# Optimization experiments

Hardware: AMD Instinct MI355X
Metric: run time of the kernel (lower is better)

The kernel has to match this reference:

```python
import jax, jax.numpy as jnp
import numpy as np

KSIZE = 11
SIGMA = 1.5
PAD = KSIZE // 2
C1 = 0.01 ** 2
C2 = 0.03 ** 2


def gaussian_kernel(ksize, sigma):
    ax = np.arange(ksize, dtype=np.float32) - (ksize - 1) / 2.0
    g = np.exp(-(ax ** 2) / (2.0 * sigma ** 2))
    k2d = np.outer(g, g)
    k2d = k2d / k2d.sum()
    # depthwise kernel for 3 channels: [out=3, in/groups=1, kh, kw]
    return jnp.asarray(np.broadcast_to(k2d, (3, 1, ksize, ksize)).copy())


def dwconv(x, kernel):
    # x: [B,3,H,W], kernel: [3,1,k,k], 'same' padding, groups=3
    return jax.lax.conv_general_dilated(
        x, kernel,
        window_strides=(1, 1),
        padding=[(PAD, PAD), (PAD, PAD)],
        dimension_numbers=('NCHW', 'OIHW', 'NCHW'),
        feature_group_count=3)


def setup_inputs() -> dict:
    key = jax.random.key(0)
    k1, k2 = jax.random.split(key)
    shape = (16, 3, 512, 512)
    img_output = jax.random.uniform(k1, shape, dtype=jnp.float32)
    img_target = jax.random.uniform(k2, shape, dtype=jnp.float32)
    kernel = gaussian_kernel(KSIZE, SIGMA)
    return {"img_output": img_output, "img_target": img_target, "kernel": kernel}


def reference(img_output, img_target, kernel):
    s, t = img_output, img_target
    ux = dwconv(s, kernel)
    uy = dwconv(t, kernel)
    uxx = dwconv(s * s, kernel)
    uyy = dwconv(t * t, kernel)
    uxy = dwconv(s * t, kernel)
    ssim = ((2 * ux * uy + C1) * (2 * (uxy - ux * uy) + C2)
            / (ux ** 2 + uy ** 2 + C1)
            / (uxx - ux * ux + (uyy - uy * uy) + C2))
    return 1.0 - ssim.mean()
```

## Files before the change

### kernel.cpp

```cpp
#include <hip/hip_runtime.h>

typedef _Float16 f16;
typedef f16  f16x8 __attribute__((ext_vector_type(8)));
typedef f16  f16x2 __attribute__((ext_vector_type(2)));
typedef float f32x4 __attribute__((ext_vector_type(4)));

#define W 512
#define H 512
#define KS 11
#define NW 4
#define NBLK 6144
#define NLINES 256
#define C1_SSIM 0.0001f
#define C2_SSIM 0.0009f
#define NTOTAL 12582912.0f

__device__ __constant__ const float GW[KS] = {
    1.02838e-3f, 7.59876e-3f, 3.600076e-2f, 1.0936069e-1f, 2.1300554e-1f,
    2.6601172e-1f,
    2.1300554e-1f, 1.0936069e-1f, 3.600076e-2f, 7.59876e-3f, 1.02838e-3f
};

union B32 { f16x2 h; int i; };

__device__ inline float ssim_px(float ux, float uy, float uxx, float uyy, float uxy) {
    const float uxuy = ux * uy;
    const float a = 2.f * uxuy + C1_SSIM;
    const float b = 2.f * (uxy - uxuy) + C2_SSIM;
    const float c = ux * ux + uy * uy + C1_SSIM;
    const float d = (uxx - ux * ux) + (uyy - uy * uy) + C2_SSIM;
    return (a * b) * __builtin_amdgcn_rcpf(c * d);
}

struct __attribute__((aligned(4))) F4 { float x, y, z, w; };

__device__ __forceinline__ void load8f(const float* __restrict__ base, int ry,
                                       int xs, float v[8]) {
    if ((unsigned)ry < (unsigned)H) {
        const float* r = base + ((size_t)ry << 9);
        if ((unsigned)xs <= (unsigned)(W - 8)) {
            const F4 a = *(const F4*)(r + xs);
            const F4 b = *(const F4*)(r + xs + 4);
            v[0] = a.x; v[1] = a.y; v[2] = a.z; v[3] = a.w;
            v[4] = b.x; v[5] = b.y; v[6] = b.z; v[7] = b.w;
        } else {
            #pragma unroll
            for (int j = 0; j < 8; ++j) {
                const int x = xs + j;
                v[j] = ((unsigned)x < (unsigned)W) ? r[x] : 0.f;
            }
        }
    } else {
        #pragma unroll
        for (int j = 0; j < 8; ++j) v[j] = 0.f;
    }
}

__device__ __forceinline__ f16x8 pack8(const float v[8]) {
    f16x8 r;
    #pragma unroll
    for (int p = 0; p < 4; ++p) {
        const f16x2 h = __builtin_bit_cast(
            f16x2, __builtin_amdgcn_cvt_pkrtz(v[2 * p], v[2 * p + 1]));
        r[2 * p]     = h[0];
        r[2 * p + 1] = h[1];
    }
    return r;
}

__global__ __launch_bounds__(256, 5)
void ssim_main(const float* __restrict__ simg, const float* __restrict__ timg,
               float* __restrict__ accum) {
    __shared__ float red[NW];

    const int tid  = threadIdx.x;
    const int w    = tid >> 6;
    const int lane = tid & 63;
    const int n    = lane & 15;
    const int q    = lane >> 4;

    const int L  = blockIdx.x * NW + w;
    const int z  = L >> 9;
    const int r  = L & 511;
    const int ty = r >> 5;
    const int tx = r & 31;

    const float* sp = simg + ((size_t)z << 18);
    const float* tp = timg + ((size_t)z << 18);
    const int x0 = tx << 4;
    const int y0 = (ty << 5) - 5;
    const int xs = x0 - 5 + (q << 3);

    f16x8 af;
    #pragma unroll
    for (int j = 0; j < 8; ++j) {
        const int k = (q << 3) + j;
        const int d = k - n;
        af[j] = (d >= 0 && d < KS) ? (f16)GW[d] : (f16)0.f;
    }

    const int LA = n | ((q & 1) << 5);
    const int LB = LA | 16;

    B32 ph[3][5][2];
    #pragma unroll
    for (int g = 0; g < 3; ++g) {
        float v[8];
        load8f(sp, y0 + (g << 4) + n, xs, v);
        const f16x8 sf = pack8(v);
        load8f(tp, y0 + (g << 4) + n, xs, v);
        const f16x8 tf = pack8(v);
        #pragma unroll
        for (int c = 0; c < 5; ++c) {
            f16x8 ch;
            if      (c == 0) ch = sf;
            else if (c == 1) ch = tf;
            else if (c == 2) ch = sf * sf;
            else if (c == 3) ch = tf * tf;
            else             ch = sf * tf;
            const f32x4 zero = {0.f, 0.f, 0.f, 0.f};
            const f32x4 d = __builtin_amdgcn_mfma_f32_16x16x32_f16(ch, af, zero, 0, 0, 0);
            ph[g][c][0].h = __builtin_bit_cast(f16x2, __builtin_amdgcn_cvt_pkrtz(d[0], d[1]));
            ph[g][c][1].h = __builtin_bit_cast(f16x2, __builtin_amdgcn_cvt_pkrtz(d[2], d[3]));
        }
    }

    float sum = 0.f;
    #pragma unroll
    for (int t = 0; t < 2; ++t) {
        f32x4 acc[5];
        #pragma unroll
        for (int c = 0; c < 5; ++c) {
            B32 a0, a1, a2, a3, b0, b1, b2, b3, r0, r1, r2, r3;
            a0.i = __shfl(ph[t][c][0].i,     LA, 64);
            a1.i = __shfl(ph[t][c][1].i,     LA, 64);
            a2.i = __shfl(ph[t][c][0].i,     LB, 64);
            a3.i = __shfl(ph[t][c][1].i,     LB, 64);
            b0.i = __shfl(ph[t + 1][c][0].i, LA, 64);
            b1.i = __shfl(ph[t + 1][c][1].i, LA, 64);
            b2.i = __shfl(ph[t + 1][c][0].i, LB, 64);
            b3.i = __shfl(ph[t + 1][c][1].i, LB, 64);
            const bool lo = (q < 2);
            r0.i = lo ? a0.i : b0.i;
            r1.i = lo ? a1.i : b1.i;
            r2.i = lo ? a2.i : b2.i;
            r3.i = lo ? a3.i : b3.i;
            f16x8 bf;
            bf[0] = r0.h[0]; bf[1] = r0.h[1];
            bf[2] = r1.h[0]; bf[3] = r1.h[1];
            bf[4] = r2.h[0]; bf[5] = r2.h[1];
            bf[6] = r3.h[0]; bf[7] = r3.h[1];
            const f32x4 zero = {0.f, 0.f, 0.f, 0.f};
            acc[c] = __builtin_amdgcn_mfma_f32_16x16x32_f16(af, bf, zero, 0, 0, 0);
        }
        #pragma unroll
        for (int rg = 0; rg < 4; ++rg)
            sum += ssim_px(acc[0][rg], acc[1][rg], acc[2][rg], acc[3][rg], acc[4][rg]);
    }

    #pragma unroll
    for (int off = 32; off > 0; off >>= 1)
        sum += __shfl_down(sum, off, 64);
    if (lane == 0) red[w] = sum;
    __syncthreads();
    if (tid == 0) {
        atomicAdd(&accum[(blockIdx.x & (NLINES - 1)) << 4],
                  red[0] + red[1] + red[2] + red[3]);
    }
}

__global__ void ssim_final(const float* __restrict__ accum, float* __restrict__ out) {
    const int lane = threadIdx.x;
    float s = 0.f;
    #pragma unroll
    for (int i = 0; i < NLINES / 64; ++i)
        s += accum[((i << 6) + lane) << 4];
    #pragma unroll
    for (int off = 32; off > 0; off >>= 1)
        s += __shfl_down(s, off, 64);
    if (lane == 0) out[0] = 1.f - s * (1.f / NTOTAL);
}

extern "C" void kernel_launch(void* const* d_in, const int* in_sizes, int n_in,
                              void* d_out, int out_size, void* d_ws, size_t ws_size,
                              hipStream_t stream) {
    const float* s = (const float*)d_in[0];
    const float* t = (const float*)d_in[1];
    float* out   = (float*)d_out;
    float* accum = (float*)d_ws;

    hipMemsetAsync(accum, 0, NLINES * 16 * sizeof(float), stream);
    ssim_main<<<dim3(NBLK), 256, 0, stream>>>(s, t, accum);
    ssim_final<<<1, 64, 0, stream>>>(accum, out);
}
```

Measured before the change: 151.7 us.

## Double tile height per wave and pipeline row-group loads with sliding MFMA passes

Each wave now covers a 16x64 output tile instead of 16x32, so there are half as many blocks. The kernel streams 5 row groups of 16 input rows through a rolling two-slot buffer. The next group's global loads are prefetched while the current group's horizontal MFMA and shuffles run, and the vertical pass for the previous pair is done as soon as both slots are ready. This cuts halo re-reads (80 input rows per 64 output rows instead of 48 per 32) and overlaps memory latency with compute. In exchange it uses more registers, lowers the occupancy hint from 5 to 4, and halves the number of blocks.

```diff
diff --git a/kernel.cpp b/kernel.cpp
--- a/kernel.cpp
+++ b/kernel.cpp
@@ -9,7 +9,7 @@
 #define H 512
 #define KS 11
 #define NW 4
-#define NBLK 6144
+#define NBLK 3072
 #define NLINES 256
 #define C1_SSIM 0.0001f
 #define C2_SSIM 0.0009f
@@ -68,7 +68,7 @@
     return r;
 }
 
-__global__ __launch_bounds__(256, 5)
+__global__ __launch_bounds__(256, 4)
 void ssim_main(const float* __restrict__ simg, const float* __restrict__ timg,
                float* __restrict__ accum) {
     __shared__ float red[NW];
@@ -80,15 +80,15 @@
     const int q    = lane >> 4;
 
     const int L  = blockIdx.x * NW + w;
-    const int z  = L >> 9;
-    const int r  = L & 511;
+    const int z  = L >> 8;
+    const int r  = L & 255;
     const int ty = r >> 5;
     const int tx = r & 31;
 
     const float* sp = simg + ((size_t)z << 18);
     const float* tp = timg + ((size_t)z << 18);
     const int x0 = tx << 4;
-    const int y0 = (ty << 5) - 5;
+    const int y0 = (ty << 6) - 5;
     const int xs = x0 - 5 + (q << 3);
 
     f16x8 af;
@@ -101,15 +101,24 @@
 
     const int LA = n | ((q & 1) << 5);
     const int LB = LA | 16;
+    const bool lo = (q < 2);
 
-    B32 ph[3][5][2];
+    float va[2][8], vb[2][8];
+    B32 sh[2][5][4];
+    float sum = 0.f;
+
+    load8f(sp, y0 + n, xs, va[0]);
+    load8f(tp, y0 + n, xs, vb[0]);
+
     #pragma unroll
-    for (int g = 0; g < 3; ++g) {
-        float v[8];
-        load8f(sp, y0 + (g << 4) + n, xs, v);
-        const f16x8 sf = pack8(v);
-        load8f(tp, y0 + (g << 4) + n, xs, v);
-        const f16x8 tf = pack8(v);
+    for (int g = 0; g < 5; ++g) {
+        const int pb = g & 1;
+        if (g < 4) {
+            load8f(sp, y0 + ((g + 1) << 4) + n, xs, va[pb ^ 1]);
+            load8f(tp, y0 + ((g + 1) << 4) + n, xs, vb[pb ^ 1]);
+        }
+        const f16x8 sf = pack8(va[pb]);
+        const f16x8 tf = pack8(vb[pb]);
         #pragma unroll
         for (int c = 0; c < 5; ++c) {
             f16x8 ch;
@@ -120,42 +129,37 @@
             else             ch = sf * tf;
             const f32x4 zero = {0.f, 0.f, 0.f, 0.f};
             const f32x4 d = __builtin_amdgcn_mfma_f32_16x16x32_f16(ch, af, zero, 0, 0, 0);
-            ph[g][c][0].h = __builtin_bit_cast(f16x2, __builtin_amdgcn_cvt_pkrtz(d[0], d[1]));
-            ph[g][c][1].h = __builtin_bit_cast(f16x2, __builtin_amdgcn_cvt_pkrtz(d[2], d[3]));
+            B32 p0, p1;
+            p0.h = __builtin_bit_cast(f16x2, __builtin_amdgcn_cvt_pkrtz(d[0], d[1]));
+            p1.h = __builtin_bit_cast(f16x2, __builtin_amdgcn_cvt_pkrtz(d[2], d[3]));
+            sh[pb][c][0].i = __shfl(p0.i, LA, 64);
+            sh[pb][c][1].i = __shfl(p1.i, LA, 64);
+            sh[pb][c][2].i = __shfl(p0.i, LB, 64);
+            sh[pb][c][3].i = __shfl(p1.i, LB, 64);
         }
-    }
-
-    float sum = 0.f;
-    #pragma unroll
-    for (int t = 0; t < 2; ++t) {
-        f32x4 acc[5];
-        #pragma unroll
-        for (int c = 0; c < 5; ++c) {
-            B32 a0, a1, a2, a3, b0, b1, b2, b3, r0, r1, r2, r3;
-            a0.i = __shfl(ph[t][c][0].i,     LA, 64);
-            a1.i = __shfl(ph[t][c][1].i,     LA, 64);
-            a2.i = __shfl(ph[t][c][0].i,     LB, 64);
-            a3.i = __shfl(ph[t][c][1].i,     LB, 64);
-            b0.i = __shfl(ph[t + 1][c][0].i, LA, 64);
-            b1.i = __shfl(ph[t + 1][c][1].i, LA, 64);
-            b2.i = __shfl(ph[t + 1][c][0].i, LB, 64);
-            b3.i = __shfl(ph[t + 1][c][1].i, LB, 64);
-            const bool lo = (q < 2);
-            r0.i = lo ? a0.i : b0.i;
-            r1.i = lo ? a1.i : b1.i;
-            r2.i = lo ? a2.i : b2.i;
-            r3.i = lo ? a3.i : b3.i;
-            f16x8 bf;
-            bf[0] = r0.h[0]; bf[1] = r0.h[1];
-            bf[2] = r1.h[0]; bf[3] = r1.h[1];
-            bf[4] = r2.h[0]; bf[5] = r2.h[1];
-            bf[6] = r3.h[0]; bf[7] = r3.h[1];
-            const f32x4 zero = {0.f, 0.f, 0.f, 0.f};
-            acc[c] = __builtin_amdgcn_mfma_f32_16x16x32_f16(af, bf, zero, 0, 0, 0);
+        if (g >= 1) {
+            const int pa = pb ^ 1;
+            f32x4 acc[5];
+            #pragma unroll
+            for (int c = 0; c < 5; ++c) {
+                B32 r0, r1, r2, r3;
+                r0.i = lo ? sh[pa][c][0].i : sh[pb][c][0].i;
+                r1.i = lo ? sh[pa][c][1].i : sh[pb][c][1].i;
+                r2.i = lo ? sh[pa][c][2].i : sh[pb][c][2].i;
+                r3.i = lo ? sh[pa][c][3].i : sh[pb][c][3].i;
+                f16x8 bf;
+                bf[0] = r0.h[0]; bf[1] = r0.h[1];
+                bf[2] = r1.h[0]; bf[3] = r1.h[1];
+                bf[4] = r2.h[0]; bf[5] = r2.h[1];
+                bf[6] = r3.h[0]; bf[7] = r3.h[1];
+                const f32x4 zero = {0.f, 0.f, 0.f, 0.f};
+                acc[c] = __builtin_amdgcn_mfma_f32_16x16x32_f16(af, bf, zero, 0, 0, 0);
+            }
+            #pragma unroll
+            for (int rg = 0; rg < 4; ++rg)
+                sum += ssim_px(acc[0][rg], acc[1][rg], acc[2][rg],
+                               acc[3][rg], acc[4][rg]);
         }
-        #pragma unroll
-        for (int rg = 0; rg < 4; ++rg)
-            sum += ssim_px(acc[0][rg], acc[1][rg], acc[2][rg], acc[3][rg], acc[4][rg]);
     }
 
     #pragma unroll
```

Measured after the change: 147.6 us. 1.03x faster.
